# Kernel optimization log

Measured on AMD Instinct MI355X. Metric: run time of the kernel, lower is better.

## Reference

```python
import jax, jax.numpy as jnp
import numpy as np

BS, L, SRC, E, H = 8, 1024, 1024, 768, 12
D = E // H  # head dim = 64


def setup_inputs() -> dict:
    key = jax.random.key(0)
    ks = jax.random.split(key, 12)
    p = lambda k, shp: (jax.random.normal(k, shp, jnp.float32) * 0.02)
    return {
        "query": jax.random.normal(ks[0], (BS, L, E), jnp.float32),
        "key": jax.random.normal(ks[1], (BS, SRC, E), jnp.float32),
        "value": jax.random.normal(ks[2], (BS, SRC, E), jnp.float32),
        "key_padding_mask": jax.random.uniform(ks[3], (BS, SRC), jnp.float32),
        "Wq": p(ks[4], (E, E)), "bq": jnp.zeros((E,), jnp.float32),
        "Wk": p(ks[5], (E, E)), "bk": jnp.zeros((E,), jnp.float32),
        "Wv": p(ks[6], (E, E)), "bv": jnp.zeros((E,), jnp.float32),
        "Wo": p(ks[7], (E, E)), "bo": jnp.zeros((E,), jnp.float32),
        "scaling_factors": jnp.array([-64, -64, -64, -32, -32, -32, -16, -16, -16, -8, -8, -8], jnp.float32),
    }


def reference(query, key, value, key_padding_mask, Wq, bq, Wk, bk, Wv, bv, Wo, bo, scaling_factors):
    bs = query.shape[0]
    # projections (torch Linear: x @ W.T + b)
    q = query @ Wq.T + bq          # [bs, L, E]
    k = key @ Wk.T + bk            # [bs, S, E]
    v = value @ Wv.T + bv          # [bs, S, E]
    # split heads
    q = q.reshape(bs, -1, H, D).transpose(0, 2, 1, 3)  # [bs, H, L, D]
    k = k.reshape(bs, -1, H, D).transpose(0, 2, 1, 3)  # [bs, H, S, D]
    v = v.reshape(bs, -1, H, D).transpose(0, 2, 1, 3)  # [bs, H, S, D]
    q = q / jnp.sqrt(jnp.float32(D))
    scores = jnp.einsum("bhld,bhsd->bhls", q, k)       # [bs, H, L, S]
    # soft key-padding bias: kpm[b,s] * scaling_factors[h]
    bias = key_padding_mask[:, None, None, :] * scaling_factors[None, :, None, None]
    scores = scores + bias
    attn = jax.nn.softmax(scores, axis=-1)             # dropout p=0 (eval)
    out = jnp.einsum("bhls,bhsd->bhld", attn, v)       # [bs, H, L, D]
    out = out.transpose(0, 2, 1, 3).reshape(bs, -1, E)  # [bs, L, E]
    return out @ Wo.T + bo
```

## Files before the change

kernel.cpp:

```cpp
#include <hip/hip_runtime.h>
#include <hip/hip_bf16.h>

typedef __attribute__((ext_vector_type(8))) short bf16x8;
typedef __attribute__((ext_vector_type(4))) float f32x4;

#define H_BS 8
#define H_L 1024
#define H_S 1024
#define H_E 768
#define H_NH 12
#define H_HD 64
#define EE (H_E * H_E)

static __device__ __forceinline__ short cvtbf(float f) {
  __hip_bfloat16 h = __float2bfloat16(f);
  return *reinterpret_cast<short*>(&h);
}

static __device__ __forceinline__ void gload16(const void* g, void* l) {
  __builtin_amdgcn_global_load_lds(
      (const __attribute__((address_space(1))) void*)g,
      (__attribute__((address_space(3))) void*)l, 16, 0, 0);
}

__global__ __launch_bounds__(256)
void conv_w4(const float* __restrict__ w0, const float* __restrict__ w1,
             const float* __restrict__ w2, const float* __restrict__ w3,
             short* __restrict__ out)
{
  const int y = blockIdx.y;
  const float* in = (y == 0) ? w0 : (y == 1) ? w1 : (y == 2) ? w2 : w3;
  short* o = out + (size_t)y * EE;
  const int i = (blockIdx.x * 256 + threadIdx.x) * 8;
  const float4 f0 = *reinterpret_cast<const float4*>(in + i);
  const float4 f1 = *reinterpret_cast<const float4*>(in + i + 4);
  bf16x8 r;
  r[0] = cvtbf(f0.x); r[1] = cvtbf(f0.y); r[2] = cvtbf(f0.z); r[3] = cvtbf(f0.w);
  r[4] = cvtbf(f1.x); r[5] = cvtbf(f1.y); r[6] = cvtbf(f1.z); r[7] = cvtbf(f1.w);
  *reinterpret_cast<bf16x8*>(o + i) = r;
}

__global__ __launch_bounds__(256)
void qkv_gemm(const float* __restrict__ Aq, const float* __restrict__ Ak,
              const float* __restrict__ Av, const short* __restrict__ Wbf,
              const float* __restrict__ bq, const float* __restrict__ bk,
              const float* __restrict__ bv, short* __restrict__ oq,
              short* __restrict__ ok_, short* __restrict__ ov)
{
  __shared__ short a_s[64][32];
  __shared__ short w_s[128][32];

  const int mode = blockIdx.z;
  const float* A    = (mode == 0) ? Aq : (mode == 1) ? Ak : Av;
  const short* W    = Wbf + (size_t)mode * EE;
  const float* bias = (mode == 0) ? bq : (mode == 1) ? bk : bv;

  const int m0 = blockIdx.y * 64;
  const int n0 = blockIdx.x * 128;
  const int t = threadIdx.x;
  const int lane = t & 63;
  const int wv = t >> 6;
  const int wm = (wv >> 1) * 32;
  const int wn = (wv & 1) * 64;
  const int lr = lane & 15;
  const int lg = lane >> 4;

  f32x4 acc[2][4];
  const f32x4 zero = {0.f, 0.f, 0.f, 0.f};
  #pragma unroll
  for (int i = 0; i < 2; ++i)
    #pragma unroll
    for (int j = 0; j < 4; ++j) acc[i][j] = zero;

  const int arow = t >> 2;
  const int acol = (t & 3) * 8;
  const float* aptr = A + (size_t)(m0 + arow) * H_E + acol;

  const int wrow = wv * 32 + (lane >> 2);
  const int wcol = (lane & 3) * 8;
  const short* wptr0 = W + (size_t)(n0 + wrow) * H_E + wcol;
  const short* wptr1 = W + (size_t)(n0 + wrow + 16) * H_E + wcol;
  short* wdst0 = &w_s[0][0] + wv * 1024;
  short* wdst1 = wdst0 + 512;

  float4 a0 = *reinterpret_cast<const float4*>(aptr);
  float4 a1 = *reinterpret_cast<const float4*>(aptr + 4);

  for (int kt = 0; kt < H_E / 32; ++kt) {
    __syncthreads();
    bf16x8 avv;
    avv[0] = cvtbf(a0.x); avv[1] = cvtbf(a0.y); avv[2] = cvtbf(a0.z); avv[3] = cvtbf(a0.w);
    avv[4] = cvtbf(a1.x); avv[5] = cvtbf(a1.y); avv[6] = cvtbf(a1.z); avv[7] = cvtbf(a1.w);
    *reinterpret_cast<bf16x8*>(&a_s[arow][acol]) = avv;
    gload16(wptr0 + kt * 32, wdst0);
    gload16(wptr1 + kt * 32, wdst1);
    __syncthreads();
    if (kt < H_E / 32 - 1) {
      a0 = *reinterpret_cast<const float4*>(aptr + (kt + 1) * 32);
      a1 = *reinterpret_cast<const float4*>(aptr + (kt + 1) * 32 + 4);
    }
    bf16x8 af[2], wf[4];
    #pragma unroll
    for (int i = 0; i < 2; ++i)
      af[i] = *reinterpret_cast<const bf16x8*>(&a_s[wm + i * 16 + lr][lg * 8]);
    #pragma unroll
    for (int j = 0; j < 4; ++j)
      wf[j] = *reinterpret_cast<const bf16x8*>(&w_s[wn + j * 16 + lr][lg * 8]);
    #pragma unroll
    for (int i = 0; i < 2; ++i)
      #pragma unroll
      for (int j = 0; j < 4; ++j)
        acc[i][j] = __builtin_amdgcn_mfma_f32_16x16x32_bf16(af[i], wf[j], acc[i][j], 0, 0, 0);
  }

  #pragma unroll
  for (int j = 0; j < 4; ++j) {
    const int gn = n0 + wn + j * 16 + lr;
    const float bvl = bias[gn];
    const int hh = gn >> 6, dd = gn & 63;
    #pragma unroll
    for (int i = 0; i < 2; ++i) {
      #pragma unroll
      for (int e = 0; e < 4; ++e) {
        const int gm = m0 + wm + i * 16 + lg * 4 + e;
        const float val = acc[i][j][e] + bvl;
        const int bb = gm >> 10, ll = gm & 1023;
        if (mode == 0)
          oq[((size_t)(bb * H_NH + hh) * H_L + ll) * H_HD + dd] = cvtbf(val * 0.125f);
        else if (mode == 1)
          ok_[((size_t)(bb * H_NH + hh) * H_S + ll) * H_HD + dd] = cvtbf(val);
        else
          ov[((size_t)(bb * H_NH + hh) * H_HD + dd) * H_S + ll] = cvtbf(val);
      }
    }
  }
}

__global__ __launch_bounds__(256)
void out_gemm(const short* __restrict__ A, const short* __restrict__ W,
              const float* __restrict__ bias, float* __restrict__ outp)
{
  __shared__ short a_s[64][32];
  __shared__ short w_s[128][32];

  const int m0 = blockIdx.y * 64;
  const int n0 = blockIdx.x * 128;
  const int t = threadIdx.x;
  const int lane = t & 63;
  const int wv = t >> 6;
  const int wm = (wv >> 1) * 32;
  const int wn = (wv & 1) * 64;
  const int lr = lane & 15;
  const int lg = lane >> 4;

  f32x4 acc[2][4];
  const f32x4 zero = {0.f, 0.f, 0.f, 0.f};
  #pragma unroll
  for (int i = 0; i < 2; ++i)
    #pragma unroll
    for (int j = 0; j < 4; ++j) acc[i][j] = zero;

  const int grow = wv * 16 + (lane >> 2);
  const int gcol = (lane & 3) * 8;
  const short* aptr = A + (size_t)(m0 + grow) * H_E + gcol;
  short* adst = &a_s[0][0] + wv * 512;

  const int wrow = wv * 32 + (lane >> 2);
  const short* wptr0 = W + (size_t)(n0 + wrow) * H_E + gcol;
  const short* wptr1 = W + (size_t)(n0 + wrow + 16) * H_E + gcol;
  short* wdst0 = &w_s[0][0] + wv * 1024;
  short* wdst1 = wdst0 + 512;

  for (int kt = 0; kt < H_E / 32; ++kt) {
    __syncthreads();
    gload16(aptr + kt * 32, adst);
    gload16(wptr0 + kt * 32, wdst0);
    gload16(wptr1 + kt * 32, wdst1);
    __syncthreads();
    bf16x8 af[2], wf[4];
    #pragma unroll
    for (int i = 0; i < 2; ++i)
      af[i] = *reinterpret_cast<const bf16x8*>(&a_s[wm + i * 16 + lr][lg * 8]);
    #pragma unroll
    for (int j = 0; j < 4; ++j)
      wf[j] = *reinterpret_cast<const bf16x8*>(&w_s[wn + j * 16 + lr][lg * 8]);
    #pragma unroll
    for (int i = 0; i < 2; ++i)
      #pragma unroll
      for (int j = 0; j < 4; ++j)
        acc[i][j] = __builtin_amdgcn_mfma_f32_16x16x32_bf16(af[i], wf[j], acc[i][j], 0, 0, 0);
  }

  #pragma unroll
  for (int j = 0; j < 4; ++j) {
    const int gn = n0 + wn + j * 16 + lr;
    const float bvl = bias[gn];
    #pragma unroll
    for (int i = 0; i < 2; ++i) {
      #pragma unroll
      for (int e = 0; e < 4; ++e) {
        const int gm = m0 + wm + i * 16 + lg * 4 + e;
        outp[(size_t)gm * H_E + gn] = acc[i][j][e] + bvl;
      }
    }
  }
}

__global__ __launch_bounds__(256)
void smha_attn(const short* __restrict__ q, const short* __restrict__ k,
               const short* __restrict__ vt, const float* __restrict__ kpm,
               const float* __restrict__ sf, short* __restrict__ outp)
{
  __shared__ short k_s[64][72];
  __shared__ short v_s[64][72];
  __shared__ short p_s[4][16][72];

  const int blk = blockIdx.x;
  const int qt = blk & 15;
  const int hh = (blk >> 4) % H_NH;
  const int bb = blk / (16 * H_NH);
  const int bh = bb * H_NH + hh;
  const int t = threadIdx.x;
  const int wv = t >> 6;
  const int lane = t & 63;
  const int lr = lane & 15;
  const int lg = lane >> 4;

  const int q0 = qt * 64 + wv * 16;

  bf16x8 qf[2];
  #pragma unroll
  for (int kk = 0; kk < 2; ++kk)
    qf[kk] = *reinterpret_cast<const bf16x8*>(
        &q[((size_t)bh * H_L + q0 + lr) * H_HD + kk * 32 + lg * 8]);

  const float sfh = sf[hh];

  f32x4 o_acc[4];
  const f32x4 zero = {0.f, 0.f, 0.f, 0.f};
  #pragma unroll
  for (int di = 0; di < 4; ++di) o_acc[di] = zero;
  float mrow[4], lrow[4];
  #pragma unroll
  for (int j = 0; j < 4; ++j) { mrow[j] = -1e30f; lrow[j] = 0.f; }

  const int srow = t >> 2;
  const int scol = (t & 3) * 16;

  const short* kp = &k[((size_t)bh * H_S + srow) * H_HD + scol];
  const short* vp = &vt[((size_t)bh * H_HD + srow) * H_S + scol];
  bf16x8 kr0 = *reinterpret_cast<const bf16x8*>(kp);
  bf16x8 kr1 = *reinterpret_cast<const bf16x8*>(kp + 8);
  bf16x8 vr0 = *reinterpret_cast<const bf16x8*>(vp);
  bf16x8 vr1 = *reinterpret_cast<const bf16x8*>(vp + 8);

  for (int kv = 0; kv < H_S / 64; ++kv) {
    const int s0 = kv * 64;
    __syncthreads();
    *reinterpret_cast<bf16x8*>(&k_s[srow][scol])     = kr0;
    *reinterpret_cast<bf16x8*>(&k_s[srow][scol + 8]) = kr1;
    *reinterpret_cast<bf16x8*>(&v_s[srow][scol])     = vr0;
    *reinterpret_cast<bf16x8*>(&v_s[srow][scol + 8]) = vr1;
    __syncthreads();
    if (kv + 1 < H_S / 64) {
      const short* kpn = kp + (size_t)(kv + 1) * 64 * H_HD;
      const short* vpn = vp + (size_t)(kv + 1) * 64;
      kr0 = *reinterpret_cast<const bf16x8*>(kpn);
      kr1 = *reinterpret_cast<const bf16x8*>(kpn + 8);
      vr0 = *reinterpret_cast<const bf16x8*>(vpn);
      vr1 = *reinterpret_cast<const bf16x8*>(vpn + 8);
    }

    float bias_c[4];
    #pragma unroll
    for (int ni = 0; ni < 4; ++ni)
      bias_c[ni] = kpm[bb * H_S + s0 + ni * 16 + lr] * sfh;

    f32x4 sc[4];
    #pragma unroll
    for (int ni = 0; ni < 4; ++ni) sc[ni] = zero;
    #pragma unroll
    for (int kk = 0; kk < 2; ++kk) {
      #pragma unroll
      for (int ni = 0; ni < 4; ++ni) {
        const bf16x8 bfr = *reinterpret_cast<const bf16x8*>(&k_s[ni * 16 + lr][kk * 32 + lg * 8]);
        sc[ni] = __builtin_amdgcn_mfma_f32_16x16x32_bf16(qf[kk], bfr, sc[ni], 0, 0, 0);
      }
    }

    #pragma unroll
    for (int j = 0; j < 4; ++j) {
      float mx = -1e30f;
      #pragma unroll
      for (int ni = 0; ni < 4; ++ni) {
        sc[ni][j] += bias_c[ni];
        mx = fmaxf(mx, sc[ni][j]);
      }
      mx = fmaxf(mx, __shfl_xor(mx, 1));
      mx = fmaxf(mx, __shfl_xor(mx, 2));
      mx = fmaxf(mx, __shfl_xor(mx, 4));
      mx = fmaxf(mx, __shfl_xor(mx, 8));
      if (!__all(mx <= mrow[j] + 8.0f)) {
        const float mnew = fmaxf(mrow[j], mx);
        const float scal = __expf(mrow[j] - mnew);
        lrow[j] *= scal;
        #pragma unroll
        for (int di = 0; di < 4; ++di) o_acc[di][j] *= scal;
        mrow[j] = mnew;
      }
      float rsum = 0.f;
      #pragma unroll
      for (int ni = 0; ni < 4; ++ni) {
        const float p = __expf(sc[ni][j] - mrow[j]);
        sc[ni][j] = p;
        rsum += p;
      }
      rsum += __shfl_xor(rsum, 1);
      rsum += __shfl_xor(rsum, 2);
      rsum += __shfl_xor(rsum, 4);
      rsum += __shfl_xor(rsum, 8);
      lrow[j] += rsum;
    }

    #pragma unroll
    for (int ni = 0; ni < 4; ++ni)
      #pragma unroll
      for (int j = 0; j < 4; ++j)
        p_s[wv][lg * 4 + j][ni * 16 + lr] = cvtbf(sc[ni][j]);

    #pragma unroll
    for (int kk = 0; kk < 2; ++kk) {
      const bf16x8 pf = *reinterpret_cast<const bf16x8*>(&p_s[wv][lr][kk * 32 + lg * 8]);
      #pragma unroll
      for (int di = 0; di < 4; ++di) {
        const bf16x8 vfr = *reinterpret_cast<const bf16x8*>(&v_s[di * 16 + lr][kk * 32 + lg * 8]);
        o_acc[di] = __builtin_amdgcn_mfma_f32_16x16x32_bf16(pf, vfr, o_acc[di], 0, 0, 0);
      }
    }
  }

  #pragma unroll
  for (int j = 0; j < 4; ++j) {
    const float rl = 1.0f / lrow[j];
    const int gq = q0 + lg * 4 + j;
    #pragma unroll
    for (int di = 0; di < 4; ++di)
      outp[((size_t)bb * H_L + gq) * H_E + hh * H_HD + di * 16 + lr] =
          cvtbf(o_acc[di][j] * rl);
  }
}

extern "C" void kernel_launch(void* const* d_in, const int* in_sizes, int n_in,
                              void* d_out, int out_size, void* d_ws, size_t ws_size,
                              hipStream_t stream)
{
  const size_t qkv = (size_t)H_BS * H_NH * H_L * H_HD;
  short* ws_w  = (short*)d_ws;
  short* ws_q  = ws_w + (size_t)4 * EE;
  short* ws_k  = ws_q + qkv;
  short* ws_vt = ws_k + qkv;
  short* ws_at = ws_vt + qkv;

  conv_w4<<<dim3(EE / 2048, 4), 256, 0, stream>>>(
      (const float*)d_in[4], (const float*)d_in[6], (const float*)d_in[8],
      (const float*)d_in[10], ws_w);

  qkv_gemm<<<dim3(H_E / 128, (H_BS * H_L) / 64, 3), 256, 0, stream>>>(
      (const float*)d_in[0], (const float*)d_in[1], (const float*)d_in[2],
      ws_w, (const float*)d_in[5], (const float*)d_in[7], (const float*)d_in[9],
      ws_q, ws_k, ws_vt);

  smha_attn<<<H_BS * H_NH * (H_L / 64), 256, 0, stream>>>(
      ws_q, ws_k, ws_vt, (const float*)d_in[3], (const float*)d_in[12], ws_at);

  out_gemm<<<dim3(H_E / 128, (H_BS * H_L) / 64), 256, 0, stream>>>(
      ws_at, ws_w + (size_t)3 * EE, (const float*)d_in[11], (float*)d_out);
}
```

Measured before the change: 332.1 us.

## Pre-convert activations to bf16 and enlarge GEMM tiles to 128x128

After: 319.3 us. 1.04x faster.

```diff
diff --git a/kernel.cpp b/kernel.cpp
--- a/kernel.cpp
+++ b/kernel.cpp
@@ -11,6 +11,7 @@
 #define H_NH 12
 #define H_HD 64
 #define EE (H_E * H_E)
+#define AN (H_BS * H_L * H_E)
 
 static __device__ __forceinline__ short cvtbf(float f) {
   __hip_bfloat16 h = __float2bfloat16(f);
@@ -24,90 +25,95 @@
 }
 
 __global__ __launch_bounds__(256)
-void conv_w4(const float* __restrict__ w0, const float* __restrict__ w1,
-             const float* __restrict__ w2, const float* __restrict__ w3,
-             short* __restrict__ out)
+void conv_bf16(const float* __restrict__ w0, const float* __restrict__ w1,
+               const float* __restrict__ w2, const float* __restrict__ w3,
+               const float* __restrict__ a0, const float* __restrict__ a1,
+               const float* __restrict__ a2,
+               short* __restrict__ ws_w, short* __restrict__ ws_a)
 {
   const int y = blockIdx.y;
-  const float* in = (y == 0) ? w0 : (y == 1) ? w1 : (y == 2) ? w2 : w3;
-  short* o = out + (size_t)y * EE;
+  const float* src;
+  short* dst;
+  int n;
+  if (y < 4) {
+    src = (y == 0) ? w0 : (y == 1) ? w1 : (y == 2) ? w2 : w3;
+    dst = ws_w + (size_t)y * EE;
+    n = EE;
+  } else {
+    src = (y == 4) ? a0 : (y == 5) ? a1 : a2;
+    dst = ws_a + (size_t)(y - 4) * AN;
+    n = AN;
+  }
   const int i = (blockIdx.x * 256 + threadIdx.x) * 8;
-  const float4 f0 = *reinterpret_cast<const float4*>(in + i);
-  const float4 f1 = *reinterpret_cast<const float4*>(in + i + 4);
+  if (i >= n) return;
+  const float4 f0 = *reinterpret_cast<const float4*>(src + i);
+  const float4 f1 = *reinterpret_cast<const float4*>(src + i + 4);
   bf16x8 r;
   r[0] = cvtbf(f0.x); r[1] = cvtbf(f0.y); r[2] = cvtbf(f0.z); r[3] = cvtbf(f0.w);
   r[4] = cvtbf(f1.x); r[5] = cvtbf(f1.y); r[6] = cvtbf(f1.z); r[7] = cvtbf(f1.w);
-  *reinterpret_cast<bf16x8*>(o + i) = r;
+  *reinterpret_cast<bf16x8*>(dst + i) = r;
 }
 
 __global__ __launch_bounds__(256)
-void qkv_gemm(const float* __restrict__ Aq, const float* __restrict__ Ak,
-              const float* __restrict__ Av, const short* __restrict__ Wbf,
+void qkv_gemm(const short* __restrict__ Abf, const short* __restrict__ Wbf,
               const float* __restrict__ bq, const float* __restrict__ bk,
               const float* __restrict__ bv, short* __restrict__ oq,
               short* __restrict__ ok_, short* __restrict__ ov)
 {
-  __shared__ short a_s[64][32];
+  __shared__ short a_s[128][32];
   __shared__ short w_s[128][32];
 
   const int mode = blockIdx.z;
-  const float* A    = (mode == 0) ? Aq : (mode == 1) ? Ak : Av;
-  const short* W    = Wbf + (size_t)mode * EE;
+  const short* A = Abf + (size_t)mode * AN;
+  const short* W = Wbf + (size_t)mode * EE;
   const float* bias = (mode == 0) ? bq : (mode == 1) ? bk : bv;
 
-  const int m0 = blockIdx.y * 64;
+  const int m0 = blockIdx.y * 128;
   const int n0 = blockIdx.x * 128;
   const int t = threadIdx.x;
   const int lane = t & 63;
   const int wv = t >> 6;
-  const int wm = (wv >> 1) * 32;
-  const int wn = (wv & 1) * 64;
+  const int wr = wv >> 1;
+  const int wc = wv & 1;
   const int lr = lane & 15;
   const int lg = lane >> 4;
 
-  f32x4 acc[2][4];
+  f32x4 acc[4][4];
   const f32x4 zero = {0.f, 0.f, 0.f, 0.f};
   #pragma unroll
-  for (int i = 0; i < 2; ++i)
+  for (int i = 0; i < 4; ++i)
     #pragma unroll
     for (int j = 0; j < 4; ++j) acc[i][j] = zero;
 
-  const int arow = t >> 2;
-  const int acol = (t & 3) * 8;
-  const float* aptr = A + (size_t)(m0 + arow) * H_E + acol;
-
-  const int wrow = wv * 32 + (lane >> 2);
-  const int wcol = (lane & 3) * 8;
-  const short* wptr0 = W + (size_t)(n0 + wrow) * H_E + wcol;
-  const short* wptr1 = W + (size_t)(n0 + wrow + 16) * H_E + wcol;
-  short* wdst0 = &w_s[0][0] + wv * 1024;
+  const int g0 = wv * 2;
+  const int srow = lane >> 2;
+  const int scol = (lane & 3) * 8;
+  const short* aptr0 = A + (size_t)(m0 + g0 * 16 + srow) * H_E + scol;
+  const short* aptr1 = aptr0 + 16 * H_E;
+  const short* wptr0 = W + (size_t)(n0 + g0 * 16 + srow) * H_E + scol;
+  const short* wptr1 = wptr0 + 16 * H_E;
+  short* adst0 = &a_s[0][0] + g0 * 512;
+  short* adst1 = adst0 + 512;
+  short* wdst0 = &w_s[0][0] + g0 * 512;
   short* wdst1 = wdst0 + 512;
 
-  float4 a0 = *reinterpret_cast<const float4*>(aptr);
-  float4 a1 = *reinterpret_cast<const float4*>(aptr + 4);
-
   for (int kt = 0; kt < H_E / 32; ++kt) {
-    __syncthreads();
-    bf16x8 avv;
-    avv[0] = cvtbf(a0.x); avv[1] = cvtbf(a0.y); avv[2] = cvtbf(a0.z); avv[3] = cvtbf(a0.w);
-    avv[4] = cvtbf(a1.x); avv[5] = cvtbf(a1.y); avv[6] = cvtbf(a1.z); avv[7] = cvtbf(a1.w);
-    *reinterpret_cast<bf16x8*>(&a_s[arow][acol]) = avv;
-    gload16(wptr0 + kt * 32, wdst0);
-    gload16(wptr1 + kt * 32, wdst1);
-    __syncthreads();
-    if (kt < H_E / 32 - 1) {
-      a0 = *reinterpret_cast<const float4*>(aptr + (kt + 1) * 32);
-      a1 = *reinterpret_cast<const float4*>(aptr + (kt + 1) * 32 + 4);
-    }
-    bf16x8 af[2], wf[4];
-    #pragma unroll
-    for (int i = 0; i < 2; ++i)
-      af[i] = *reinterpret_cast<const bf16x8*>(&a_s[wm + i * 16 + lr][lg * 8]);
+    const int ko = kt * 32;
+    __syncthreads();
+    gload16(aptr0 + ko, adst0);
+    gload16(aptr1 + ko, adst1);
+    gload16(wptr0 + ko, wdst0);
+    gload16(wptr1 + ko, wdst1);
+    __syncthreads();
+    bf16x8 af[4], wf[4];
+    #pragma unroll
+    for (int i = 0; i < 4; ++i)
+      af[i] = *reinterpret_cast<const bf16x8*>(&a_s[wr * 64 + i * 16 + lr][lg * 8]);
     #pragma unroll
     for (int j = 0; j < 4; ++j)
-      wf[j] = *reinterpret_cast<const bf16x8*>(&w_s[wn + j * 16 + lr][lg * 8]);
-    #pragma unroll
-    for (int i = 0; i < 2; ++i)
+      wf[j] = *reinterpret_cast<const bf16x8*>(&w_s[wc * 64 + j * 16 + lr][lg * 8]);
+    #pragma unroll
+    for (int i = 0; i < 4; ++i)
       #pragma unroll
       for (int j = 0; j < 4; ++j)
         acc[i][j] = __builtin_amdgcn_mfma_f32_16x16x32_bf16(af[i], wf[j], acc[i][j], 0, 0, 0);
@@ -115,14 +121,14 @@
 
   #pragma unroll
   for (int j = 0; j < 4; ++j) {
-    const int gn = n0 + wn + j * 16 + lr;
+    const int gn = n0 + wc * 64 + j * 16 + lr;
     const float bvl = bias[gn];
     const int hh = gn >> 6, dd = gn & 63;
     #pragma unroll
-    for (int i = 0; i < 2; ++i) {
+    for (int i = 0; i < 4; ++i) {
       #pragma unroll
       for (int e = 0; e < 4; ++e) {
-        const int gm = m0 + wm + i * 16 + lg * 4 + e;
+        const int gm = m0 + wr * 64 + i * 16 + lg * 4 + e;
         const float val = acc[i][j][e] + bvl;
         const int bb = gm >> 10, ll = gm & 1023;
         if (mode == 0)
@@ -140,52 +146,55 @@
 void out_gemm(const short* __restrict__ A, const short* __restrict__ W,
               const float* __restrict__ bias, float* __restrict__ outp)
 {
-  __shared__ short a_s[64][32];
+  __shared__ short a_s[128][32];
   __shared__ short w_s[128][32];
 
-  const int m0 = blockIdx.y * 64;
+  const int m0 = blockIdx.y * 128;
   const int n0 = blockIdx.x * 128;
   const int t = threadIdx.x;
   const int lane = t & 63;
   const int wv = t >> 6;
-  const int wm = (wv >> 1) * 32;
-  const int wn = (wv & 1) * 64;
+  const int wr = wv >> 1;
+  const int wc = wv & 1;
   const int lr = lane & 15;
   const int lg = lane >> 4;
 
-  f32x4 acc[2][4];
+  f32x4 acc[4][4];
   const f32x4 zero = {0.f, 0.f, 0.f, 0.f};
   #pragma unroll
-  for (int i = 0; i < 2; ++i)
+  for (int i = 0; i < 4; ++i)
     #pragma unroll
     for (int j = 0; j < 4; ++j) acc[i][j] = zero;
 
-  const int grow = wv * 16 + (lane >> 2);
-  const int gcol = (lane & 3) * 8;
-  const short* aptr = A + (size_t)(m0 + grow) * H_E + gcol;
-  short* adst = &a_s[0][0] + wv * 512;
-
-  const int wrow = wv * 32 + (lane >> 2);
-  const short* wptr0 = W + (size_t)(n0 + wrow) * H_E + gcol;
-  const short* wptr1 = W + (size_t)(n0 + wrow + 16) * H_E + gcol;
-  short* wdst0 = &w_s[0][0] + wv * 1024;
+  const int g0 = wv * 2;
+  const int srow = lane >> 2;
+  const int scol = (lane & 3) * 8;
+  const short* aptr0 = A + (size_t)(m0 + g0 * 16 + srow) * H_E + scol;
+  const short* aptr1 = aptr0 + 16 * H_E;
+  const short* wptr0 = W + (size_t)(n0 + g0 * 16 + srow) * H_E + scol;
+  const short* wptr1 = wptr0 + 16 * H_E;
+  short* adst0 = &a_s[0][0] + g0 * 512;
+  short* adst1 = adst0 + 512;
+  short* wdst0 = &w_s[0][0] + g0 * 512;
   short* wdst1 = wdst0 + 512;
 
   for (int kt = 0; kt < H_E / 32; ++kt) {
-    __syncthreads();
-    gload16(aptr + kt * 32, adst);
-    gload16(wptr0 + kt * 32, wdst0);
-    gload16(wptr1 + kt * 32, wdst1);
-    __syncthreads();
-    bf16x8 af[2], wf[4];
-    #pragma unroll
-    for (int i = 0; i < 2; ++i)
-      af[i] = *reinterpret_cast<const bf16x8*>(&a_s[wm + i * 16 + lr][lg * 8]);
+    const int ko = kt * 32;
+    __syncthreads();
+    gload16(aptr0 + ko, adst0);
+    gload16(aptr1 + ko, adst1);
+    gload16(wptr0 + ko, wdst0);
+    gload16(wptr1 + ko, wdst1);
+    __syncthreads();
+    bf16x8 af[4], wf[4];
+    #pragma unroll
+    for (int i = 0; i < 4; ++i)
+      af[i] = *reinterpret_cast<const bf16x8*>(&a_s[wr * 64 + i * 16 + lr][lg * 8]);
     #pragma unroll
     for (int j = 0; j < 4; ++j)
-      wf[j] = *reinterpret_cast<const bf16x8*>(&w_s[wn + j * 16 + lr][lg * 8]);
-    #pragma unroll
-    for (int i = 0; i < 2; ++i)
+      wf[j] = *reinterpret_cast<const bf16x8*>(&w_s[wc * 64 + j * 16 + lr][lg * 8]);
+    #pragma unroll
+    for (int i = 0; i < 4; ++i)
       #pragma unroll
       for (int j = 0; j < 4; ++j)
         acc[i][j] = __builtin_amdgcn_mfma_f32_16x16x32_bf16(af[i], wf[j], acc[i][j], 0, 0, 0);
@@ -193,13 +202,13 @@
 
   #pragma unroll
   for (int j = 0; j < 4; ++j) {
-    const int gn = n0 + wn + j * 16 + lr;
+    const int gn = n0 + wc * 64 + j * 16 + lr;
     const float bvl = bias[gn];
     #pragma unroll
-    for (int i = 0; i < 2; ++i) {
+    for (int i = 0; i < 4; ++i) {
       #pragma unroll
       for (int e = 0; e < 4; ++e) {
-        const int gm = m0 + wm + i * 16 + lg * 4 + e;
+        const int gm = m0 + wr * 64 + i * 16 + lg * 4 + e;
         outp[(size_t)gm * H_E + gn] = acc[i][j][e] + bvl;
       }
     }
@@ -354,25 +363,25 @@
                               void* d_out, int out_size, void* d_ws, size_t ws_size,
                               hipStream_t stream)
 {
-  const size_t qkv = (size_t)H_BS * H_NH * H_L * H_HD;
   short* ws_w  = (short*)d_ws;
-  short* ws_q  = ws_w + (size_t)4 * EE;
-  short* ws_k  = ws_q + qkv;
-  short* ws_vt = ws_k + qkv;
-  short* ws_at = ws_vt + qkv;
-
-  conv_w4<<<dim3(EE / 2048, 4), 256, 0, stream>>>(
+  short* ws_a  = ws_w + (size_t)4 * EE;
+  short* ws_q  = ws_a + (size_t)3 * AN;
+  short* ws_k  = ws_q + AN;
+  short* ws_vt = ws_k + AN;
+  short* ws_at = ws_a;
+
+  conv_bf16<<<dim3(AN / 2048, 7), 256, 0, stream>>>(
       (const float*)d_in[4], (const float*)d_in[6], (const float*)d_in[8],
-      (const float*)d_in[10], ws_w);
-
-  qkv_gemm<<<dim3(H_E / 128, (H_BS * H_L) / 64, 3), 256, 0, stream>>>(
-      (const float*)d_in[0], (const float*)d_in[1], (const float*)d_in[2],
-      ws_w, (const float*)d_in[5], (const float*)d_in[7], (const float*)d_in[9],
-      ws_q, ws_k, ws_vt);
+      (const float*)d_in[10], (const float*)d_in[0], (const float*)d_in[1],
+      (const float*)d_in[2], ws_w, ws_a);
+
+  qkv_gemm<<<dim3(H_E / 128, (H_BS * H_L) / 128, 3), 256, 0, stream>>>(
+      ws_a, ws_w, (const float*)d_in[5], (const float*)d_in[7],
+      (const float*)d_in[9], ws_q, ws_k, ws_vt);
 
   smha_attn<<<H_BS * H_NH * (H_L / 64), 256, 0, stream>>>(
       ws_q, ws_k, ws_vt, (const float*)d_in[3], (const float*)d_in[12], ws_at);
 
-  out_gemm<<<dim3(H_E / 128, (H_BS * H_L) / 64), 256, 0, stream>>>(
+  out_gemm<<<dim3(H_E / 128, (H_BS * H_L) / 128), 256, 0, stream>>>(
       ws_at, ws_w + (size_t)3 * EE, (const float*)d_in[11], (float*)d_out);
 }
```
